# Kernel tuning notes

Measured on AMD Instinct MI355X. Metric: run time of the kernel, lower is better.

Reference implementation:

```python
import jax, jax.numpy as jnp
import numpy as np


def _conv2d(x, w, stride, padding):
    # x: NCHW, w: OIHW
    return jax.lax.conv_general_dilated(
        x, w, window_strides=(stride, stride),
        padding=((padding, padding), (padding, padding)),
        dimension_numbers=('NCHW', 'OIHW', 'NCHW'))


def setup_inputs() -> dict:
    key = jax.random.key(0)
    k1, k2 = jax.random.split(key)
    B, C_in, H, Wd = 8, 64, 256, 256
    C_out, ksz = 64, 3
    x = jax.random.normal(k1, (B, C_in, H, Wd), dtype=jnp.float32)
    W = jax.random.normal(k2, (C_out, C_in, ksz, ksz), dtype=jnp.float32)
    b = jnp.zeros((C_out,), dtype=jnp.float32)
    return {"x": x, "W": W, "b": b}


def reference(x, W, b):
    stride, padding = 1, 1
    B, C, H, Wd = x.shape
    # per-pixel (across-channel) normalization of activations
    xf = jnp.transpose(x, (0, 2, 3, 1)).reshape(-1, C)       # [B*H*W, C]
    mu = jnp.mean(xf, axis=-1, keepdims=True)
    var = jnp.mean((xf - mu) ** 2, axis=-1, keepdims=True)    # unbiased=False
    r = 1.0 / jnp.sqrt(var + 1e-8)
    y_norm = r * (xf - mu)
    # int8 fake-quant per pixel
    s_act = 127.0 / jnp.maximum(jnp.max(jnp.abs(y_norm), axis=-1, keepdims=True), 1e-8)
    y_tilde = jnp.clip(jnp.round(s_act * y_norm), -128.0, 127.0) / s_act
    y4 = jnp.transpose(y_tilde.reshape(B, H, Wd, C), (0, 3, 1, 2))
    # ternary weight quant (value; STE only matters for backward)
    s_w = 1.0 / jnp.maximum(jnp.mean(jnp.abs(W)), 1e-8)
    w_tilde = jnp.clip(jnp.round(s_w * W), -1.0, 1.0) / s_w
    out = _conv2d(y4, w_tilde, stride, padding) + b[None, :, None, None]
    return out
```

## Files before the change

### kernel.cpp

```cpp
#include <hip/hip_runtime.h>

typedef _Float16 half8 __attribute__((ext_vector_type(8)));
typedef float    f32x4 __attribute__((ext_vector_type(4)));

#define NB   8
#define NC   64
#define NH   256
#define NW   256
#define NO   64
#define TW_OFF   0ull
#define TW_BYTES (576ull * 64ull * 2ull)
#define MSW_OFF  (TW_OFF + TW_BYTES)
#define PART_OFF (MSW_OFF + 16ull)

__global__ __launch_bounds__(256) void wsum_kernel(const float* __restrict__ W,
                                                   float* __restrict__ partial) {
    __shared__ float red[256];
    int tid = threadIdx.x;
    red[tid] = fabsf(W[blockIdx.x * 256 + tid]);
    __syncthreads();
    for (int off = 128; off > 0; off >>= 1) {
        if (tid < off) red[tid] += red[tid + off];
        __syncthreads();
    }
    if (tid == 0) partial[blockIdx.x] = red[0];
}

__global__ __launch_bounds__(256) void wq2_kernel(const float* __restrict__ W,
                                                  const float* __restrict__ partial,
                                                  _Float16* __restrict__ tw2,
                                                  float* __restrict__ msw_out) {
    __shared__ float red[256];
    int tid = threadIdx.x;
    red[tid] = (tid < 144) ? partial[tid] : 0.0f;
    __syncthreads();
    for (int off = 128; off > 0; off >>= 1) {
        if (tid < off) red[tid] += red[tid + off];
        __syncthreads();
    }
    float mean = red[0] / 36864.0f;
    float msw  = fmaxf(mean, 1e-8f);
    float s_w  = 1.0f / msw;
    if (blockIdx.x == 0 && tid == 0) msw_out[0] = msw;

    int idx = blockIdx.x * 256 + tid;
    float t = rintf(s_w * W[idx]);
    t = fminf(1.0f, fmaxf(-1.0f, t));
    int o  = idx / 576;
    int r  = idx - o * 576;
    int c  = r / 9;
    int r2 = r - c * 9;
    int kh = r2 / 3;
    int kw = r2 - kh * 3;
    int k  = (kh * 3 + kw) * 64 + c;
    tw2[((k >> 3) * 64 + o) * 8 + (k & 7)] = (_Float16)t;
}

__global__ __launch_bounds__(256, 4) void fused_kernel(const float* __restrict__ x,
                                                       const _Float16* __restrict__ tw2,
                                                       const float* __restrict__ msw_p,
                                                       const float* __restrict__ bias,
                                                       float* __restrict__ out) {
    __shared__ alignas(16) _Float16 lds[3 * 8 * 66 * 8];

    int tid = threadIdx.x;
    int pb  = blockIdx.x;
    int bid = (pb & 7) * 1024 + (pb >> 3);
    int wt = bid & 3;
    int h  = (bid >> 2) & 255;
    int bb = bid >> 10;
    int w0 = wt * 64;

    if (tid < 198) {
        int kh = tid / 66;
        int wl = tid - kh * 66;
        int hp = h + kh - 1;
        int wp = w0 + wl - 1;
        int inb = ((unsigned)hp < 256u) & ((unsigned)wp < 256u);
        int hpc = min(max(hp, 0), 255);
        int wpc = min(max(wp, 0), 255);
        const float* xp = x + (size_t)bb * 64 * 65536 + (size_t)hpc * 256 + wpc;
        float fin = (float)inb;

        float s = 0.0f, sq = 0.0f, mn = 1e30f, mx = -1e30f;
        #pragma unroll
        for (int cc = 0; cc < 8; ++cc) {
            half8 hv;
            #pragma unroll
            for (int j = 0; j < 8; ++j) {
                float v = xp[(size_t)(cc * 8 + j) * 65536] * fin;
                s  += v;
                sq += v * v;
                mn = fminf(mn, v);
                mx = fmaxf(mx, v);
                hv[j] = (_Float16)v;
            }
            *(half8*)(lds + ((kh * 8 + cc) * 66 + wl) * 8) = hv;
        }
        float mu  = s * (1.0f / 64.0f);
        float var = fmaxf(sq * (1.0f / 64.0f) - mu * mu, 0.0f);
        float r    = 1.0f / sqrtf(var + 1e-8f);
        float dmax = fmaxf(mx - mu, mu - mn);
        float amax = fmaxf(dmax * r, 1e-8f);
        float s_a  = 127.0f / amax;
        float invs = amax / 127.0f;

        #pragma unroll
        for (int cc = 0; cc < 8; ++cc) {
            half8 hv = *(half8*)(lds + ((kh * 8 + cc) * 66 + wl) * 8);
            #pragma unroll
            for (int j = 0; j < 8; ++j) {
                float yn = ((float)hv[j] - mu) * r;
                float q  = rintf(s_a * yn);
                q = fminf(127.0f, fmaxf(-128.0f, q));
                hv[j] = (_Float16)(q * invs);
            }
            *(half8*)(lds + ((kh * 8 + cc) * 66 + wl) * 8) = hv;
        }
    }

    int l   = tid & 63;
    int wv  = tid >> 6;
    int l15 = l & 15;
    int q8  = l >> 4;

    half8 aw[18];
    #pragma unroll
    for (int ks = 0; ks < 18; ++ks)
        aw[ks] = *(const half8*)(tw2 + (((ks * 4 + q8) * 64) + wv * 16 + l15) * 8);

    __syncthreads();

    f32x4 acc[4];
    #pragma unroll
    for (int nt = 0; nt < 4; ++nt)
        #pragma unroll
        for (int r2 = 0; r2 < 4; ++r2) acc[nt][r2] = 0.0f;

    #pragma unroll
    for (int ks = 0; ks < 18; ++ks) {
        int tap = ks >> 1;
        int kh  = tap / 3;
        int kw  = tap - kh * 3;
        int ccb = (ks & 1) * 4 + q8;
        int base = ((kh * 8 + ccb) * 66 + kw + l15) * 8;
        #pragma unroll
        for (int nt = 0; nt < 4; ++nt) {
            half8 bf = *(const half8*)(lds + base + nt * 128);
            acc[nt] = __builtin_amdgcn_mfma_f32_16x16x32_f16(aw[ks], bf, acc[nt], 0, 0, 0);
        }
    }

    float msw = *msw_p;
    size_t obase = ((size_t)bb * 64) * 65536 + (size_t)h * 256;
    #pragma unroll
    for (int reg = 0; reg < 4; ++reg) {
        int o = wv * 16 + q8 * 4 + reg;
        float bo = bias[o];
        #pragma unroll
        for (int nt = 0; nt < 4; ++nt) {
            int w = w0 + nt * 16 + l15;
            out[obase + (size_t)o * 65536 + w] = acc[nt][reg] * msw + bo;
        }
    }
}

extern "C" void kernel_launch(void* const* d_in, const int* in_sizes, int n_in,
                              void* d_out, int out_size, void* d_ws, size_t ws_size,
                              hipStream_t stream) {
    const float* x = (const float*)d_in[0];
    const float* W = (const float*)d_in[1];
    const float* b = (const float*)d_in[2];
    float* out = (float*)d_out;

    char* ws = (char*)d_ws;
    _Float16* tw2  = (_Float16*)(ws + TW_OFF);
    float*    msw  = (float*)(ws + MSW_OFF);
    float*    part = (float*)(ws + PART_OFF);

    wsum_kernel<<<144, 256, 0, stream>>>(W, part);
    wq2_kernel<<<144, 256, 0, stream>>>(W, part, tw2, msw);
    fused_kernel<<<8192, 256, 0, stream>>>(x, tw2, msw, b, out);
}
```

Baseline: 313.5 us.

## Compute four output rows per block to reuse normalized input halo rows

```diff
diff --git a/kernel.cpp b/kernel.cpp
--- a/kernel.cpp
+++ b/kernel.cpp
@@ -8,6 +8,7 @@
 #define NH   256
 #define NW   256
 #define NO   64
+#define HT   4
 #define TW_OFF   0ull
 #define TW_BYTES (576ull * 64ull * 2ull)
 #define MSW_OFF  (TW_OFF + TW_BYTES)
@@ -56,31 +57,38 @@
     tw2[((k >> 3) * 64 + o) * 8 + (k & 7)] = (_Float16)t;
 }
 
-__global__ __launch_bounds__(256, 4) void fused_kernel(const float* __restrict__ x,
+__global__ __launch_bounds__(256, 3) void fused_kernel(const float* __restrict__ x,
                                                        const _Float16* __restrict__ tw2,
                                                        const float* __restrict__ msw_p,
                                                        const float* __restrict__ bias,
                                                        float* __restrict__ out) {
-    __shared__ alignas(16) _Float16 lds[3 * 8 * 66 * 8];
+    __shared__ alignas(16) _Float16 lds[6 * 8 * 66 * 8];
 
     int tid = threadIdx.x;
     int pb  = blockIdx.x;
-    int bid = (pb & 7) * 1024 + (pb >> 3);
+    int bid = (pb & 7) * 256 + (pb >> 3);
     int wt = bid & 3;
-    int h  = (bid >> 2) & 255;
-    int bb = bid >> 10;
+    int ht = (bid >> 2) & 63;
+    int bb = bid >> 8;
+    int h0 = ht * HT;
     int w0 = wt * 64;
 
-    if (tid < 198) {
-        int kh = tid / 66;
-        int wl = tid - kh * 66;
-        int hp = h + kh - 1;
+    for (int p = tid; p < 396; p += 256) {
+        int kh = p / 66;
+        int wl = p - kh * 66;
+        int hp = h0 + kh - 1;
         int wp = w0 + wl - 1;
-        int inb = ((unsigned)hp < 256u) & ((unsigned)wp < 256u);
-        int hpc = min(max(hp, 0), 255);
-        int wpc = min(max(wp, 0), 255);
-        const float* xp = x + (size_t)bb * 64 * 65536 + (size_t)hpc * 256 + wpc;
-        float fin = (float)inb;
+        _Float16* slot = lds + kh * 4224 + wl * 8;
+
+        if (((unsigned)hp >= 256u) | ((unsigned)wp >= 256u)) {
+            half8 z;
+            #pragma unroll
+            for (int j = 0; j < 8; ++j) z[j] = (_Float16)0.0f;
+            #pragma unroll
+            for (int cc = 0; cc < 8; ++cc) *(half8*)(slot + cc * 528) = z;
+            continue;
+        }
+        const float* xp = x + (size_t)bb * 4194304 + (size_t)hp * 256 + wp;
 
         float s = 0.0f, sq = 0.0f, mn = 1e30f, mx = -1e30f;
         #pragma unroll
@@ -88,14 +96,14 @@
             half8 hv;
             #pragma unroll
             for (int j = 0; j < 8; ++j) {
-                float v = xp[(size_t)(cc * 8 + j) * 65536] * fin;
+                float v = xp[(size_t)(cc * 8 + j) * 65536];
                 s  += v;
                 sq += v * v;
                 mn = fminf(mn, v);
                 mx = fmaxf(mx, v);
                 hv[j] = (_Float16)v;
             }
-            *(half8*)(lds + ((kh * 8 + cc) * 66 + wl) * 8) = hv;
+            *(half8*)(slot + cc * 528) = hv;
         }
         float mu  = s * (1.0f / 64.0f);
         float var = fmaxf(sq * (1.0f / 64.0f) - mu * mu, 0.0f);
@@ -104,18 +112,19 @@
         float amax = fmaxf(dmax * r, 1e-8f);
         float s_a  = 127.0f / amax;
         float invs = amax / 127.0f;
+        float af   = s_a * r;
+        float bf   = -mu * af;
 
         #pragma unroll
         for (int cc = 0; cc < 8; ++cc) {
-            half8 hv = *(half8*)(lds + ((kh * 8 + cc) * 66 + wl) * 8);
+            half8 hv = *(half8*)(slot + cc * 528);
             #pragma unroll
             for (int j = 0; j < 8; ++j) {
-                float yn = ((float)hv[j] - mu) * r;
-                float q  = rintf(s_a * yn);
+                float q = rintf(fmaf((float)hv[j], af, bf));
                 q = fminf(127.0f, fmaxf(-128.0f, q));
                 hv[j] = (_Float16)(q * invs);
             }
-            *(half8*)(lds + ((kh * 8 + cc) * 66 + wl) * 8) = hv;
+            *(half8*)(slot + cc * 528) = hv;
         }
     }
 
@@ -131,36 +140,39 @@
 
     __syncthreads();
 
-    f32x4 acc[4];
+    float msw = *msw_p;
     #pragma unroll
-    for (int nt = 0; nt < 4; ++nt)
+    for (int r = 0; r < HT; ++r) {
+        f32x4 acc[4];
         #pragma unroll
-        for (int r2 = 0; r2 < 4; ++r2) acc[nt][r2] = 0.0f;
+        for (int nt = 0; nt < 4; ++nt)
+            #pragma unroll
+            for (int r2 = 0; r2 < 4; ++r2) acc[nt][r2] = 0.0f;
 
-    #pragma unroll
-    for (int ks = 0; ks < 18; ++ks) {
-        int tap = ks >> 1;
-        int kh  = tap / 3;
-        int kw  = tap - kh * 3;
-        int ccb = (ks & 1) * 4 + q8;
-        int base = ((kh * 8 + ccb) * 66 + kw + l15) * 8;
         #pragma unroll
-        for (int nt = 0; nt < 4; ++nt) {
-            half8 bf = *(const half8*)(lds + base + nt * 128);
-            acc[nt] = __builtin_amdgcn_mfma_f32_16x16x32_f16(aw[ks], bf, acc[nt], 0, 0, 0);
+        for (int ks = 0; ks < 18; ++ks) {
+            int tap = ks >> 1;
+            int kh  = tap / 3;
+            int kw  = tap - kh * 3;
+            int ccb = (ks & 1) * 4 + q8;
+            int base = (((kh + r) * 8 + ccb) * 66 + kw + l15) * 8;
+            #pragma unroll
+            for (int nt = 0; nt < 4; ++nt) {
+                half8 bf = *(const half8*)(lds + base + nt * 128);
+                acc[nt] = __builtin_amdgcn_mfma_f32_16x16x32_f16(aw[ks], bf, acc[nt], 0, 0, 0);
+            }
         }
-    }
 
-    float msw = *msw_p;
-    size_t obase = ((size_t)bb * 64) * 65536 + (size_t)h * 256;
-    #pragma unroll
-    for (int reg = 0; reg < 4; ++reg) {
-        int o = wv * 16 + q8 * 4 + reg;
-        float bo = bias[o];
+        size_t obase = ((size_t)bb * 64) * 65536 + (size_t)(h0 + r) * 256;
         #pragma unroll
-        for (int nt = 0; nt < 4; ++nt) {
-            int w = w0 + nt * 16 + l15;
-            out[obase + (size_t)o * 65536 + w] = acc[nt][reg] * msw + bo;
+        for (int reg = 0; reg < 4; ++reg) {
+            int o = wv * 16 + q8 * 4 + reg;
+            float bo = bias[o];
+            #pragma unroll
+            for (int nt = 0; nt < 4; ++nt) {
+                int w = w0 + nt * 16 + l15;
+                out[obase + (size_t)o * 65536 + w] = acc[nt][reg] * msw + bo;
+            }
         }
     }
 }
@@ -180,5 +192,5 @@
 
     wsum_kernel<<<144, 256, 0, stream>>>(W, part);
     wq2_kernel<<<144, 256, 0, stream>>>(W, part, tw2, msw);
-    fused_kernel<<<8192, 256, 0, stream>>>(x, tw2, msw, b, out);
+    fused_kernel<<<2048, 256, 0, stream>>>(x, tw2, msw, b, out);
 }
```

Measured after the change: 285.0 us. 9.1% less time.
